# Kernel optimization log

Measured on AMD Instinct MI355X. Metric: run time of the kernel, lower is better.

## Reference

```python
import jax, jax.numpy as jnp
import numpy as np

B, N, D, L = 32, 1024, 128, 2  # batch graphs, nodes, hidden dim, num GIN layers
BN_EPS = 1e-5


def _batchnorm(x2d, gamma, beta):
    # Training-mode BatchNorm1d over flattened (B*N, D) with biased variance
    mean = jnp.mean(x2d, axis=0)
    var = jnp.mean(jnp.square(x2d - mean), axis=0)
    return (x2d - mean) * (gamma / jnp.sqrt(var + BN_EPS)) + beta


def setup_inputs() -> dict:
    key = jax.random.key(0)
    ks = jax.random.split(key, 12)
    s = 1.0 / np.sqrt(D)  # torch Linear default init scale
    inp = {
        "x": jax.random.normal(ks[0], (B, N, D), dtype=jnp.float32),
        "padded_nei": jax.random.randint(ks[1], (B, N, 8), 0, N, dtype=jnp.int64),
        "adj": jax.random.uniform(ks[2], (B, N, N), dtype=jnp.float32),
        # stacked per-layer params [L, ...]
        "W1": jax.random.uniform(ks[3], (L, D, D), jnp.float32, -s, s),
        "b1": jax.random.uniform(ks[4], (L, D), jnp.float32, -s, s),
        "W2": jax.random.uniform(ks[5], (L, D, D), jnp.float32, -s, s),
        "b2": jax.random.uniform(ks[6], (L, D), jnp.float32, -s, s),
        "g_in": jnp.ones((L, D), jnp.float32),   # MLP-internal BN gamma
        "be_in": jnp.zeros((L, D), jnp.float32),  # MLP-internal BN beta
        "g_out": jnp.ones((L, D), jnp.float32),  # GraphCNN outer BN gamma
        "be_out": jnp.zeros((L, D), jnp.float32),
    }
    return inp


def reference(x, padded_nei, adj, W1, b1, W2, b2, g_in, be_in, g_out, be_out):
    h = x  # [B, N, D]
    for l in range(L):
        # sum-pooling over neighbors via batched dense adjacency matmul
        pooled = jnp.einsum('bij,bjd->bid', adj, h)  # [B, N, D]
        # MLP: Linear -> BN -> ReLU -> Linear
        z = pooled @ W1[l] + b1[l]
        z = jax.nn.relu(_batchnorm(z.reshape(-1, D), g_in[l], be_in[l])).reshape(B, N, D)
        z = z @ W2[l] + b2[l]
        # outer BatchNorm1d + ReLU
        h = jax.nn.relu(_batchnorm(z.reshape(-1, D), g_out[l], be_out[l])).reshape(B, N, D)
    return h
```

## Files before the change

### kernel.cpp

```cpp
#include <hip/hip_runtime.h>
#include <stdint.h>


#define BB 32
#define NN 1024
#define DD 128
#define RR 32768

typedef __bf16 bf16_t;
typedef bf16_t bf16x8 __attribute__((ext_vector_type(8)));
typedef unsigned short us8 __attribute__((ext_vector_type(8)));
typedef float f32x4 __attribute__((ext_vector_type(4)));

__device__ __forceinline__ unsigned short f2b(float f) {
  unsigned u = __float_as_uint(f);
  u += 0x7fff + ((u >> 16) & 1);
  return (unsigned short)(u >> 16);
}
__device__ __forceinline__ float b2f(unsigned short s) {
  return __uint_as_float((unsigned)s << 16);
}

#define GLL(GP, LP)                                              \
  __builtin_amdgcn_global_load_lds(                              \
      (const __attribute__((address_space(1))) void*)(GP),       \
      (__attribute__((address_space(3))) void*)(LP), 16, 0, 0)

__global__ __launch_bounds__(256) void k0_prep(const float* __restrict__ x,
                                               const float* __restrict__ adj,
                                               const float* __restrict__ W1,
                                               const float* __restrict__ W2,
                                               unsigned short* __restrict__ hT,
                                               unsigned short* __restrict__ W1T,
                                               unsigned short* __restrict__ W2T,
                                               unsigned short* __restrict__ adjB,
                                               float* __restrict__ stats) {
  const int tid = threadIdx.x;
  if (blockIdx.x >= 512) {
    size_t i8 = ((size_t)(blockIdx.x - 512) * 256 + tid) * 8;
    float4 a = *(const float4*)(adj + i8);
    float4 b = *(const float4*)(adj + i8 + 4);
    alignas(16) unsigned short t[8] = {f2b(a.x), f2b(a.y), f2b(a.z), f2b(a.w),
                                       f2b(b.x), f2b(b.y), f2b(b.z), f2b(b.w)};
    *(uint4*)(adjB + i8) = *(const uint4*)t;
    return;
  }
  if (blockIdx.x < 256) {
    const int b = blockIdx.x >> 3, nt = blockIdx.x & 7;
    __shared__ alignas(16) unsigned short T[128][136];
    const int r = tid >> 1, c0 = (tid & 1) * 64;
    const float* src = x + ((size_t)(b * 8 + nt) * 128 + r) * 128 + c0;
#pragma unroll
    for (int i = 0; i < 64; i += 4) {
      float4 v = *(const float4*)(src + i);
      int c = c0 + i;
      T[c][r] = f2b(v.x); T[c + 1][r] = f2b(v.y);
      T[c + 2][r] = f2b(v.z); T[c + 3][r] = f2b(v.w);
    }
    __syncthreads();
    const int d = tid >> 1, n0 = (tid & 1) * 64;
    unsigned short* dst = hT + ((size_t)b * DD + d) * NN + nt * 128 + n0;
#pragma unroll
    for (int i = 0; i < 64; i += 8)
      *(uint4*)(dst + i) = *(const uint4*)&T[d][n0 + i];
  } else {
    if (blockIdx.x == 256) {
      stats[tid] = 0.f; stats[256 + tid] = 0.f;
      stats[512 + tid] = 0.f; stats[768 + tid] = 0.f;
    }
    int idx = (blockIdx.x - 256) * 256 + tid;
    int w = idx >> 15;
    int rem = idx & 32767;
    int l = rem >> 14;
    int n = (rem >> 7) & 127;
    int k = rem & 127;
    const float* W = w ? W2 : W1;
    unsigned short* WT = w ? W2T : W1T;
    WT[((size_t)l * 128 + n) * 128 + k] = f2b(W[((size_t)l * 128 + k) * 128 + n]);
  }
}

__global__ __launch_bounds__(256, 1) void kA_pool_lin(
    const unsigned short* __restrict__ adjB, const unsigned short* __restrict__ hT,
    const unsigned short* __restrict__ WT, const float* __restrict__ bias,
    unsigned short* __restrict__ z1b, float* __restrict__ gsum,
    float* __restrict__ gsq) {
  const int blk = blockIdx.x;
  const int b = (blk & 7) | ((blk >> 6) << 3);
  const int mt = (blk >> 3) & 7;
  const int tid = threadIdx.x;
  const int wave = tid >> 6, lane = tid & 63;
  const int wc = wave * 32;
  const int ln = lane & 15, q = lane >> 4;

  __shared__ union {
    struct {
      unsigned short A[3][8192];
      unsigned short B[3][8192];
    } s;
    unsigned short As2[128][136];
  } sm;

  const unsigned short* adjb = adjB + ((size_t)b * NN + mt * 128) * NN;
  const unsigned short* hTb = hT + (size_t)b * DD * NN;

  const int srow = tid >> 3;
  const int sseg = (((tid & 7) ^ (srow & 7)) << 3);
  const unsigned short* gA = adjb + (size_t)srow * NN + sseg;
  const unsigned short* gB = hTb + (size_t)srow * NN + sseg;

#define STAGE(P, K0)                                \
  do {                                              \
    unsigned short* ap = sm.s.A[(P)];               \
    unsigned short* bp = sm.s.B[(P)];               \
    GLL(gA + (K0), ap + tid * 8);                   \
    GLL(gA + 32 * NN + (K0), ap + 2048 + tid * 8);  \
    GLL(gA + 64 * NN + (K0), ap + 4096 + tid * 8);  \
    GLL(gA + 96 * NN + (K0), ap + 6144 + tid * 8);  \
    GLL(gB + (K0), bp + tid * 8);                   \
    GLL(gB + 32 * NN + (K0), bp + 2048 + tid * 8);  \
    GLL(gB + 64 * NN + (K0), bp + 4096 + tid * 8);  \
    GLL(gB + 96 * NN + (K0), bp + 6144 + tid * 8);  \
  } while (0)

  STAGE(0, 0);
  STAGE(1, 64);
  STAGE(2, 128);

  f32x4 acc1[8][2];
  f32x4 zero = {0.f, 0.f, 0.f, 0.f};
#pragma unroll
  for (int i = 0; i < 8; i++) { acc1[i][0] = zero; acc1[i][1] = zero; }

  const int xorv = (ln & 7) << 4;

#pragma unroll
  for (int t = 0; t < 16; ++t) {
    const int p = t % 3;
    if (t < 14)
      asm volatile("s_waitcnt vmcnt(16)" ::: "memory");
    else if (t == 14)
      asm volatile("s_waitcnt vmcnt(8)" ::: "memory");
    else
      asm volatile("s_waitcnt vmcnt(0)" ::: "memory");
    __builtin_amdgcn_s_barrier();
    __builtin_amdgcn_sched_barrier(0);
    {
      const char* Ab = (const char*)sm.s.A[p];
      const char* Bb = (const char*)sm.s.B[p];
#pragma unroll
      for (int kk = 0; kk < 2; kk++) {
        const int co = ((kk << 6) + (q << 4)) ^ xorv;
        bf16x8 af[8], bfr[2];
#pragma unroll
        for (int i = 0; i < 8; i++)
          af[i] = *(const bf16x8*)(Ab + (i * 16 + ln) * 128 + co);
#pragma unroll
        for (int j = 0; j < 2; j++)
          bfr[j] = *(const bf16x8*)(Bb + (wc + j * 16 + ln) * 128 + co);
#pragma unroll
        for (int i = 0; i < 8; i++)
#pragma unroll
          for (int j = 0; j < 2; j++)
            acc1[i][j] = __builtin_amdgcn_mfma_f32_16x16x32_bf16(af[i], bfr[j], acc1[i][j], 0, 0, 0);
      }
    }
    __builtin_amdgcn_sched_barrier(0);
    __builtin_amdgcn_s_barrier();
    __builtin_amdgcn_sched_barrier(0);
    if (t < 13) STAGE(p, (t + 3) * 64);
  }
#undef STAGE

#pragma unroll
  for (int i = 0; i < 8; i++) {
    int row = i * 16 + q * 4;
#pragma unroll
    for (int j = 0; j < 2; j++) {
      int col = wc + j * 16 + ln;
#pragma unroll
      for (int r = 0; r < 4; r++) sm.As2[row + r][col] = f2b(acc1[i][j][r]);
    }
  }
  __syncthreads();

  f32x4 acc2[8][2];
#pragma unroll
  for (int i = 0; i < 8; i++) { acc2[i][0] = zero; acc2[i][1] = zero; }
#pragma unroll
  for (int ks = 0; ks < 4; ks++) {
    bf16x8 af[8], wf[2];
#pragma unroll
    for (int i = 0; i < 8; i++)
      af[i] = *(const bf16x8*)&sm.As2[i * 16 + ln][ks * 32 + q * 8];
#pragma unroll
    for (int j = 0; j < 2; j++)
      wf[j] = *(const bf16x8*)&WT[(size_t)(wc + j * 16 + ln) * 128 + ks * 32 + q * 8];
#pragma unroll
    for (int i = 0; i < 8; i++)
#pragma unroll
      for (int j = 0; j < 2; j++)
        acc2[i][j] = __builtin_amdgcn_mfma_f32_16x16x32_bf16(af[i], wf[j], acc2[i][j], 0, 0, 0);
  }

  const size_t row0 = (size_t)b * NN + mt * 128;
#pragma unroll
  for (int j = 0; j < 2; j++) {
    int col = wc + j * 16 + ln;
    float bc = bias[col];
    float s1 = 0.f, s2 = 0.f;
#pragma unroll
    for (int i = 0; i < 8; i++) {
      int row = i * 16 + q * 4;
#pragma unroll
      for (int r = 0; r < 4; r++) {
        float v = acc2[i][j][r] + bc;
        z1b[(row0 + row + r) * 128 + col] = f2b(v);
        s1 += v; s2 += v * v;
      }
    }
    s1 += __shfl_xor(s1, 16); s1 += __shfl_xor(s1, 32);
    s2 += __shfl_xor(s2, 16); s2 += __shfl_xor(s2, 32);
    if (q == 0) { atomicAdd(&gsum[col], s1); atomicAdd(&gsq[col], s2); }
  }
}

__global__ __launch_bounds__(256, 2) void kB_lin(
    const unsigned short* __restrict__ Zin, const float* __restrict__ gsum_in,
    const float* __restrict__ gsq_in, const float* __restrict__ gamma,
    const float* __restrict__ beta, const unsigned short* __restrict__ WT,
    const float* __restrict__ bias, unsigned short* __restrict__ z2b,
    float* __restrict__ gsum, float* __restrict__ gsq) {
  const int mt = blockIdx.x;
  const int tid = threadIdx.x;
  const int wave = tid >> 6, lane = tid & 63;
  const int wc = wave * 32;
  const int ln = lane & 15, q = lane >> 4;

  __shared__ alignas(16) unsigned short Az[64 * 128];
  __shared__ float nsc[128], nsh[128];

  bf16x8 wfr[4][2];
#pragma unroll
  for (int ks = 0; ks < 4; ks++)
#pragma unroll
    for (int j = 0; j < 2; j++)
      wfr[ks][j] = *(const bf16x8*)&WT[(size_t)(wc + j * 16 + ln) * 128 + ks * 32 + q * 8];

  const size_t row0 = (size_t)mt * 64;
  const int rZ = tid >> 4;
  const int uZ = (((tid & 15) ^ (rZ & 7)) << 3);
  const unsigned short* gZ = Zin + (row0 + rZ) * 128 + uZ;
  GLL(gZ, Az + tid * 8);
  GLL(gZ + 16 * 128, Az + 2048 + tid * 8);
  GLL(gZ + 32 * 128, Az + 4096 + tid * 8);
  GLL(gZ + 48 * 128, Az + 6144 + tid * 8);

  if (tid < 128) {
    float mean = gsum_in[tid] * (1.f / 32768.f);
    float var = gsq_in[tid] * (1.f / 32768.f) - mean * mean;
    float sc = gamma[tid] * rsqrtf(var + 1e-5f);
    nsc[tid] = sc; nsh[tid] = beta[tid] - mean * sc;
  }
  __syncthreads();

  f32x4 acc[4][2];
  f32x4 zero = {0.f, 0.f, 0.f, 0.f};
#pragma unroll
  for (int i = 0; i < 4; i++) { acc[i][0] = zero; acc[i][1] = zero; }

  const int xorv = (ln & 7) << 4;
#pragma unroll
  for (int ks = 0; ks < 4; ks++) {
    bf16x8 af[4];
#pragma unroll
    for (int i = 0; i < 4; i++) {
      us8 raw = *(const us8*)((const char*)Az + (i * 16 + ln) * 256 +
                              (((ks << 6) + (q << 4)) ^ xorv));
      us8 t;
#pragma unroll
      for (int e = 0; e < 8; e++) {
        int col = ks * 32 + q * 8 + e;
        t[e] = f2b(fmaxf(fmaf(b2f(raw[e]), nsc[col], nsh[col]), 0.f));
      }
      af[i] = *(bf16x8*)&t;
    }
#pragma unroll
    for (int i = 0; i < 4; i++)
#pragma unroll
      for (int j = 0; j < 2; j++)
        acc[i][j] = __builtin_amdgcn_mfma_f32_16x16x32_bf16(af[i], wfr[ks][j], acc[i][j], 0, 0, 0);
  }

#pragma unroll
  for (int j = 0; j < 2; j++) {
    int col = wc + j * 16 + ln;
    float bc = bias[col];
    float s1 = 0.f, s2 = 0.f;
#pragma unroll
    for (int i = 0; i < 4; i++) {
      int row = i * 16 + q * 4;
#pragma unroll
      for (int r = 0; r < 4; r++) {
        float v = acc[i][j][r] + bc;
        z2b[(row0 + row + r) * 128 + col] = f2b(v);
        s1 += v; s2 += v * v;
      }
    }
    s1 += __shfl_xor(s1, 16); s1 += __shfl_xor(s1, 32);
    s2 += __shfl_xor(s2, 16); s2 += __shfl_xor(s2, 32);
    if (q == 0) { atomicAdd(&gsum[col], s1); atomicAdd(&gsq[col], s2); }
  }
}

__global__ __launch_bounds__(256) void k4_bnt(const unsigned short* __restrict__ Z,
                                              const float* __restrict__ gsum,
                                              const float* __restrict__ gsq,
                                              const float* __restrict__ gamma,
                                              const float* __restrict__ beta,
                                              unsigned short* __restrict__ hT) {
  const int b = blockIdx.x, nt = blockIdx.y, tid = threadIdx.x;
  __shared__ alignas(16) unsigned short T[128][136];
  __shared__ float nsc[128], nsh[128];
  if (tid < 128) {
    float mean = gsum[tid] * (1.f / 32768.f);
    float var = gsq[tid] * (1.f / 32768.f) - mean * mean;
    float sc = gamma[tid] * rsqrtf(var + 1e-5f);
    nsc[tid] = sc; nsh[tid] = beta[tid] - mean * sc;
  }
  __syncthreads();
  const int r = tid >> 1, c0 = (tid & 1) * 64;
  const unsigned short* src = Z + ((size_t)(b * 8 + nt) * 128 + r) * 128 + c0;
#pragma unroll
  for (int u = 0; u < 8; u++) {
    uint4 raw = *(const uint4*)(src + u * 8);
    const unsigned short* s = (const unsigned short*)&raw;
#pragma unroll
    for (int e = 0; e < 8; e++) {
      int c = c0 + u * 8 + e;
      T[c][r] = f2b(fmaxf(fmaf(b2f(s[e]), nsc[c], nsh[c]), 0.f));
    }
  }
  __syncthreads();
  const int d = tid >> 1, n0 = (tid & 1) * 64;
  unsigned short* dst = hT + ((size_t)b * DD + d) * NN + nt * 128 + n0;
#pragma unroll
  for (int i = 0; i < 64; i += 8)
    *(uint4*)(dst + i) = *(const uint4*)&T[d][n0 + i];
}

__global__ __launch_bounds__(256) void k4_out(const unsigned short* __restrict__ Z,
                                              const float* __restrict__ gsum,
                                              const float* __restrict__ gsq,
                                              const float* __restrict__ gamma,
                                              const float* __restrict__ beta,
                                              float* __restrict__ out) {
  const int blk = blockIdx.x, tid = threadIdx.x;
  __shared__ float nsc[128], nsh[128];
  if (tid < 128) {
    float mean = gsum[tid] * (1.f / 32768.f);
    float var = gsq[tid] * (1.f / 32768.f) - mean * mean;
    float sc = gamma[tid] * rsqrtf(var + 1e-5f);
    nsc[tid] = sc; nsh[tid] = beta[tid] - mean * sc;
  }
  __syncthreads();
  const int r = tid >> 1, c0 = (tid & 1) * 64;
  const unsigned short* src = Z + ((size_t)blk * 128 + r) * 128 + c0;
  float* dst = out + ((size_t)blk * 128 + r) * 128 + c0;
#pragma unroll
  for (int u = 0; u < 8; u++) {
    uint4 raw = *(const uint4*)(src + u * 8);
    const unsigned short* s = (const unsigned short*)&raw;
    float4 o;
    int c = c0 + u * 8;
    o.x = fmaxf(fmaf(b2f(s[0]), nsc[c], nsh[c]), 0.f);
    o.y = fmaxf(fmaf(b2f(s[1]), nsc[c + 1], nsh[c + 1]), 0.f);
    o.z = fmaxf(fmaf(b2f(s[2]), nsc[c + 2], nsh[c + 2]), 0.f);
    o.w = fmaxf(fmaf(b2f(s[3]), nsc[c + 3], nsh[c + 3]), 0.f);
    *(float4*)(dst + u * 8) = o;
    o.x = fmaxf(fmaf(b2f(s[4]), nsc[c + 4], nsh[c + 4]), 0.f);
    o.y = fmaxf(fmaf(b2f(s[5]), nsc[c + 5], nsh[c + 5]), 0.f);
    o.z = fmaxf(fmaf(b2f(s[6]), nsc[c + 6], nsh[c + 6]), 0.f);
    o.w = fmaxf(fmaf(b2f(s[7]), nsc[c + 7], nsh[c + 7]), 0.f);
    *(float4*)(dst + u * 8 + 4) = o;
  }
}

extern "C" void kernel_launch(void* const* d_in, const int* in_sizes, int n_in,
                              void* d_out, int out_size, void* d_ws, size_t ws_size,
                              hipStream_t stream) {
  const float* x = (const float*)d_in[0];
  const float* adj = (const float*)d_in[2];
  const float* W1 = (const float*)d_in[3];
  const float* b1 = (const float*)d_in[4];
  const float* W2 = (const float*)d_in[5];
  const float* b2 = (const float*)d_in[6];
  const float* g_in = (const float*)d_in[7];
  const float* be_in = (const float*)d_in[8];
  const float* g_out = (const float*)d_in[9];
  const float* be_out = (const float*)d_in[10];
  float* out = (float*)d_out;

  char* ws = (char*)d_ws;
  unsigned short* hT = (unsigned short*)ws;
  unsigned short* z1b = (unsigned short*)(ws + 8ull * 1024 * 1024);
  unsigned short* z2b = (unsigned short*)(ws + 16ull * 1024 * 1024);
  unsigned short* W1T = (unsigned short*)(ws + 24ull * 1024 * 1024);
  unsigned short* W2T = W1T + 2 * 128 * 128;
  float* stats = (float*)(ws + 25ull * 1024 * 1024);
  unsigned short* adjB = (unsigned short*)(ws + 26ull * 1024 * 1024);

  k0_prep<<<512 + 16384, 256, 0, stream>>>(x, adj, W1, W2, hT, W1T, W2T, adjB,
                                           stats);

  for (int l = 0; l < 2; l++) {
    float* st_in = stats + (l * 2 + 0) * 256;
    float* st_out = stats + (l * 2 + 1) * 256;
    kA_pool_lin<<<256, 256, 0, stream>>>(adjB, hT, W1T + l * 16384,
                                         b1 + l * 128, z1b, st_in,
                                         st_in + 128);
    kB_lin<<<512, 256, 0, stream>>>(z1b, st_in, st_in + 128, g_in + l * 128,
                                    be_in + l * 128, W2T + l * 16384,
                                    b2 + l * 128, z2b, st_out, st_out + 128);
    if (l == 0)
      k4_bnt<<<dim3(32, 8), 256, 0, stream>>>(z2b, st_out, st_out + 128, g_out,
                                              be_out, hT);
    else
      k4_out<<<256, 256, 0, stream>>>(z2b, st_out, st_out + 128, g_out + 128,
                                      be_out + 128, out);
  }
}
```

Before: 333.2 us.

## Use 8-wave blocks in pooled GEMM and grid-stride the adjacency conversion

The pooling+linear kernel now runs 512 threads per block, and its 8 waves split the 128x128 output tile 2x4 instead of 4 column strips. Each wave holds half as many accumulators, and each thread issues half as many LDS-staging loads, with the vmcnt waits adjusted to match. This is meant to raise latency hiding and MFMA issue per CU. Separately, the adj fp32->bf16 conversion uses 2048 blocks, each looping 8 times, instead of 16384 single-shot blocks, to cut block launch overhead.

Measured after the change: 352.4 us. 5.8% more time.

```diff
diff --git a/kernel.cpp b/kernel.cpp
--- a/kernel.cpp
+++ b/kernel.cpp
@@ -37,12 +37,16 @@
                                                float* __restrict__ stats) {
   const int tid = threadIdx.x;
   if (blockIdx.x >= 512) {
-    size_t i8 = ((size_t)(blockIdx.x - 512) * 256 + tid) * 8;
-    float4 a = *(const float4*)(adj + i8);
-    float4 b = *(const float4*)(adj + i8 + 4);
-    alignas(16) unsigned short t[8] = {f2b(a.x), f2b(a.y), f2b(a.z), f2b(a.w),
-                                       f2b(b.x), f2b(b.y), f2b(b.z), f2b(b.w)};
-    *(uint4*)(adjB + i8) = *(const uint4*)t;
+    const int bid = blockIdx.x - 512;
+#pragma unroll
+    for (int it = 0; it < 8; ++it) {
+      size_t i8 = (((size_t)it * 2048 + bid) * 256 + tid) * 8;
+      float4 a = *(const float4*)(adj + i8);
+      float4 b = *(const float4*)(adj + i8 + 4);
+      alignas(16) unsigned short t[8] = {f2b(a.x), f2b(a.y), f2b(a.z), f2b(a.w),
+                                         f2b(b.x), f2b(b.y), f2b(b.z), f2b(b.w)};
+      *(uint4*)(adjB + i8) = *(const uint4*)t;
+    }
     return;
   }
   if (blockIdx.x < 256) {
@@ -80,7 +84,7 @@
   }
 }
 
-__global__ __launch_bounds__(256, 1) void kA_pool_lin(
+__global__ __launch_bounds__(512, 1) void kA_pool_lin(
     const unsigned short* __restrict__ adjB, const unsigned short* __restrict__ hT,
     const unsigned short* __restrict__ WT, const float* __restrict__ bias,
     unsigned short* __restrict__ z1b, float* __restrict__ gsum,
@@ -90,7 +94,8 @@
   const int mt = (blk >> 3) & 7;
   const int tid = threadIdx.x;
   const int wave = tid >> 6, lane = tid & 63;
-  const int wc = wave * 32;
+  const int wr = wave >> 2;
+  const int wn = wave & 3;
   const int ln = lane & 15, q = lane >> 4;
 
   __shared__ union {
@@ -104,33 +109,29 @@
   const unsigned short* adjb = adjB + ((size_t)b * NN + mt * 128) * NN;
   const unsigned short* hTb = hT + (size_t)b * DD * NN;
 
-  const int srow = tid >> 3;
-  const int sseg = (((tid & 7) ^ (srow & 7)) << 3);
-  const unsigned short* gA = adjb + (size_t)srow * NN + sseg;
-  const unsigned short* gB = hTb + (size_t)srow * NN + sseg;
+  const int r0 = tid >> 3, c0s = (((tid & 7) ^ (r0 & 7)) << 3);
+  const int r1 = (tid + 512) >> 3, c1s = ((((tid + 512) & 7) ^ (r1 & 7)) << 3);
+  const unsigned short* gA0 = adjb + (size_t)r0 * NN + c0s;
+  const unsigned short* gA1 = adjb + (size_t)r1 * NN + c1s;
+  const unsigned short* gB0 = hTb + (size_t)r0 * NN + c0s;
+  const unsigned short* gB1 = hTb + (size_t)r1 * NN + c1s;
 
 #define STAGE(P, K0)                                \
   do {                                              \
-    unsigned short* ap = sm.s.A[(P)];               \
-    unsigned short* bp = sm.s.B[(P)];               \
-    GLL(gA + (K0), ap + tid * 8);                   \
-    GLL(gA + 32 * NN + (K0), ap + 2048 + tid * 8);  \
-    GLL(gA + 64 * NN + (K0), ap + 4096 + tid * 8);  \
-    GLL(gA + 96 * NN + (K0), ap + 6144 + tid * 8);  \
-    GLL(gB + (K0), bp + tid * 8);                   \
-    GLL(gB + 32 * NN + (K0), bp + 2048 + tid * 8);  \
-    GLL(gB + 64 * NN + (K0), bp + 4096 + tid * 8);  \
-    GLL(gB + 96 * NN + (K0), bp + 6144 + tid * 8);  \
+    GLL(gA0 + (K0), sm.s.A[(P)] + tid * 8);         \
+    GLL(gA1 + (K0), sm.s.A[(P)] + 4096 + tid * 8);  \
+    GLL(gB0 + (K0), sm.s.B[(P)] + tid * 8);         \
+    GLL(gB1 + (K0), sm.s.B[(P)] + 4096 + tid * 8);  \
   } while (0)
 
   STAGE(0, 0);
   STAGE(1, 64);
   STAGE(2, 128);
 
-  f32x4 acc1[8][2];
+  f32x4 acc1[4][2];
   f32x4 zero = {0.f, 0.f, 0.f, 0.f};
 #pragma unroll
-  for (int i = 0; i < 8; i++) { acc1[i][0] = zero; acc1[i][1] = zero; }
+  for (int i = 0; i < 4; i++) { acc1[i][0] = zero; acc1[i][1] = zero; }
 
   const int xorv = (ln & 7) << 4;
 
@@ -138,9 +139,9 @@
   for (int t = 0; t < 16; ++t) {
     const int p = t % 3;
     if (t < 14)
-      asm volatile("s_waitcnt vmcnt(16)" ::: "memory");
+      asm volatile("s_waitcnt vmcnt(8)" ::: "memory");
     else if (t == 14)
-      asm volatile("s_waitcnt vmcnt(8)" ::: "memory");
+      asm volatile("s_waitcnt vmcnt(4)" ::: "memory");
     else
       asm volatile("s_waitcnt vmcnt(0)" ::: "memory");
     __builtin_amdgcn_s_barrier();
@@ -151,15 +152,15 @@
 #pragma unroll
       for (int kk = 0; kk < 2; kk++) {
         const int co = ((kk << 6) + (q << 4)) ^ xorv;
-        bf16x8 af[8], bfr[2];
-#pragma unroll
-        for (int i = 0; i < 8; i++)
-          af[i] = *(const bf16x8*)(Ab + (i * 16 + ln) * 128 + co);
+        bf16x8 af[4], bfr[2];
+#pragma unroll
+        for (int i = 0; i < 4; i++)
+          af[i] = *(const bf16x8*)(Ab + (wr * 64 + i * 16 + ln) * 128 + co);
 #pragma unroll
         for (int j = 0; j < 2; j++)
-          bfr[j] = *(const bf16x8*)(Bb + (wc + j * 16 + ln) * 128 + co);
-#pragma unroll
-        for (int i = 0; i < 8; i++)
+          bfr[j] = *(const bf16x8*)(Bb + (wn * 32 + j * 16 + ln) * 128 + co);
+#pragma unroll
+        for (int i = 0; i < 4; i++)
 #pragma unroll
           for (int j = 0; j < 2; j++)
             acc1[i][j] = __builtin_amdgcn_mfma_f32_16x16x32_bf16(af[i], bfr[j], acc1[i][j], 0, 0, 0);
@@ -173,31 +174,31 @@
 #undef STAGE
 
 #pragma unroll
-  for (int i = 0; i < 8; i++) {
-    int row = i * 16 + q * 4;
+  for (int i = 0; i < 4; i++) {
+    int row = wr * 64 + i * 16 + q * 4;
 #pragma unroll
     for (int j = 0; j < 2; j++) {
-      int col = wc + j * 16 + ln;
+      int col = wn * 32 + j * 16 + ln;
 #pragma unroll
       for (int r = 0; r < 4; r++) sm.As2[row + r][col] = f2b(acc1[i][j][r]);
     }
   }
   __syncthreads();
 
-  f32x4 acc2[8][2];
-#pragma unroll
-  for (int i = 0; i < 8; i++) { acc2[i][0] = zero; acc2[i][1] = zero; }
+  f32x4 acc2[4][2];
+#pragma unroll
+  for (int i = 0; i < 4; i++) { acc2[i][0] = zero; acc2[i][1] = zero; }
 #pragma unroll
   for (int ks = 0; ks < 4; ks++) {
-    bf16x8 af[8], wf[2];
-#pragma unroll
-    for (int i = 0; i < 8; i++)
-      af[i] = *(const bf16x8*)&sm.As2[i * 16 + ln][ks * 32 + q * 8];
+    bf16x8 af[4], wf[2];
+#pragma unroll
+    for (int i = 0; i < 4; i++)
+      af[i] = *(const bf16x8*)&sm.As2[wr * 64 + i * 16 + ln][ks * 32 + q * 8];
 #pragma unroll
     for (int j = 0; j < 2; j++)
-      wf[j] = *(const bf16x8*)&WT[(size_t)(wc + j * 16 + ln) * 128 + ks * 32 + q * 8];
-#pragma unroll
-    for (int i = 0; i < 8; i++)
+      wf[j] = *(const bf16x8*)&WT[(size_t)(wn * 32 + j * 16 + ln) * 128 + ks * 32 + q * 8];
+#pragma unroll
+    for (int i = 0; i < 4; i++)
 #pragma unroll
       for (int j = 0; j < 2; j++)
         acc2[i][j] = __builtin_amdgcn_mfma_f32_16x16x32_bf16(af[i], wf[j], acc2[i][j], 0, 0, 0);
@@ -206,12 +207,12 @@
   const size_t row0 = (size_t)b * NN + mt * 128;
 #pragma unroll
   for (int j = 0; j < 2; j++) {
-    int col = wc + j * 16 + ln;
+    int col = wn * 32 + j * 16 + ln;
     float bc = bias[col];
     float s1 = 0.f, s2 = 0.f;
 #pragma unroll
-    for (int i = 0; i < 8; i++) {
-      int row = i * 16 + q * 4;
+    for (int i = 0; i < 4; i++) {
+      int row = wr * 64 + i * 16 + q * 4;
 #pragma unroll
       for (int r = 0; r < 4; r++) {
         float v = acc2[i][j][r] + bc;
@@ -410,13 +411,13 @@
   float* stats = (float*)(ws + 25ull * 1024 * 1024);
   unsigned short* adjB = (unsigned short*)(ws + 26ull * 1024 * 1024);
 
-  k0_prep<<<512 + 16384, 256, 0, stream>>>(x, adj, W1, W2, hT, W1T, W2T, adjB,
-                                           stats);
+  k0_prep<<<512 + 2048, 256, 0, stream>>>(x, adj, W1, W2, hT, W1T, W2T, adjB,
+                                          stats);
 
   for (int l = 0; l < 2; l++) {
     float* st_in = stats + (l * 2 + 0) * 256;
     float* st_out = stats + (l * 2 + 1) * 256;
-    kA_pool_lin<<<256, 256, 0, stream>>>(adjB, hT, W1T + l * 16384,
+    kA_pool_lin<<<256, 512, 0, stream>>>(adjB, hT, W1T + l * 16384,
                                          b1 + l * 128, z1b, st_in,
                                          st_in + 128);
     kB_lin<<<512, 256, 0, stream>>>(z1b, st_in, st_in + 128, g_in + l * 128,
```
